# Kernel tuning notes

Measured on AMD Instinct MI355X. Metric: run time of the kernel, lower is better.

## Reference

```python
import jax, jax.numpy as jnp
import numpy as np
import math

FOV, NEAR, FAR = 60.0, 0.1, 100.0
W_RES, H_RES = 128, 128
N_GAUSS = 1024


def _normalize(v):
    return v / (jnp.linalg.norm(v) + 1e-8)


def _view_matrix(pos, look_at, up):
    # Same construction as Camera._compute_view_matrix
    f = _normalize(look_at - pos)
    r = _normalize(jnp.cross(f, up))
    u = _normalize(jnp.cross(r, f))
    return jnp.stack([
        jnp.concatenate([r, -jnp.dot(r, pos)[None]]),
        jnp.concatenate([u, -jnp.dot(u, pos)[None]]),
        jnp.concatenate([-f, jnp.dot(f, pos)[None]]),
        jnp.array([0.0, 0.0, 0.0, 1.0], dtype=pos.dtype),
    ])


def _proj_matrix():
    # Same construction as Camera._compute_projection_matrix
    aspect = W_RES / H_RES
    foc = 1.0 / math.tan(math.radians(FOV) / 2.0)
    P = np.zeros((4, 4), np.float32)
    P[0, 0] = foc / aspect
    P[1, 1] = foc
    P[2, 2] = (FAR + NEAR) / (NEAR - FAR)
    P[2, 3] = 2.0 * FAR * NEAR / (NEAR - FAR)
    P[3, 2] = -1.0
    return jnp.asarray(P)


def _quat_to_rot(q):
    # q: [N,4] (w,x,y,z) -> [N,3,3]
    q = q / (jnp.linalg.norm(q, axis=-1, keepdims=True) + 1e-8)
    w, x, y, z = q[:, 0], q[:, 1], q[:, 2], q[:, 3]
    return jnp.stack([
        jnp.stack([1 - 2 * (y * y + z * z), 2 * (x * y - w * z), 2 * (x * z + w * y)], -1),
        jnp.stack([2 * (x * y + w * z), 1 - 2 * (x * x + z * z), 2 * (y * z - w * x)], -1),
        jnp.stack([2 * (x * z - w * y), 2 * (y * z + w * x), 1 - 2 * (x * x + y * y)], -1),
    ], axis=1)


def _splat(means, log_scales, quats, opacity_logits, colors, cam_position, look_at, up):
    V = _view_matrix(cam_position, look_at, up)
    P = _proj_matrix()

    # 3D covariance: R S S^T R^T
    R = _quat_to_rot(quats)                       # [N,3,3]
    S = jnp.exp(log_scales)                       # [N,3]
    M = R * S[:, None, :]
    cov3d = jnp.einsum('nij,nkj->nik', M, M)      # [N,3,3]

    # Project means to view / clip / pixel space
    mh = jnp.concatenate([means, jnp.ones((means.shape[0], 1), means.dtype)], -1)
    pv = mh @ V.T                                 # [N,4] view space
    tx, ty, tz = pv[:, 0], pv[:, 1], pv[:, 2]     # tz < 0 in front of camera
    depth = -tz
    clip = pv @ P.T
    cw = jnp.where(jnp.abs(clip[:, 3]) < 1e-6, 1e-6, clip[:, 3])
    ndc = clip[:, :2] / cw[:, None]
    px = (ndc[:, 0] + 1.0) * 0.5 * W_RES          # pixel x center
    py = (ndc[:, 1] + 1.0) * 0.5 * H_RES          # pixel y center

    # EWA Jacobian -> 2D covariance
    foc = 1.0 / math.tan(math.radians(FOV) / 2.0)
    fx = foc / (W_RES / H_RES) * (W_RES / 2.0)
    fy = foc * (H_RES / 2.0)
    zsafe = jnp.where(jnp.abs(tz) < 1e-6, 1e-6, tz)
    zero = jnp.zeros_like(zsafe)
    J = jnp.stack([
        jnp.stack([fx / zsafe, zero, -fx * tx / (zsafe * zsafe)], -1),
        jnp.stack([zero, fy / zsafe, -fy * ty / (zsafe * zsafe)], -1),
    ], axis=1)                                    # [N,2,3]
    T = jnp.einsum('nij,jk->nik', J, V[:3, :3])   # [N,2,3]
    cov2d = jnp.einsum('nij,njk,nlk->nil', T, cov3d, T)  # [N,2,2]
    a = cov2d[:, 0, 0] + 0.3
    b = cov2d[:, 0, 1]
    c = cov2d[:, 1, 1] + 0.3
    det = jnp.maximum(a * c - b * b, 1e-6)
    ia, ib, ic = c / det, -b / det, a / det       # inverse 2x2

    # Per-pixel Gaussian weights: [N,H,W]
    u = jnp.arange(W_RES, dtype=means.dtype) + 0.5
    v = jnp.arange(H_RES, dtype=means.dtype) + 0.5
    dx = px[:, None, None] - u[None, None, :]
    dy = py[:, None, None] - v[None, :, None]
    power = -0.5 * (ia[:, None, None] * dx * dx
                    + 2.0 * ib[:, None, None] * dx * dy
                    + ic[:, None, None] * dy * dy)
    opac = jax.nn.sigmoid(opacity_logits)
    w = opac[:, None, None] * jnp.exp(jnp.minimum(power, 0.0))
    valid = (depth > NEAR) & (depth < FAR)
    w = jnp.where(valid[:, None, None], w, 0.0)
    w = jnp.clip(w, 0.0, 0.99)

    # Depth sort (front-to-back) then alpha composite via exclusive cumsum of log(1-a)
    order = jnp.argsort(depth)
    ws = w[order]                                 # [N,H,W]
    cs = jax.nn.sigmoid(colors)[order]            # [N,3]
    ds = depth[order]
    log_om = jnp.log1p(-ws)
    trans = jnp.exp(jnp.cumsum(log_om, axis=0) - log_om)  # exclusive transmittance
    contrib = trans * ws                          # [N,H,W]
    rgb = jnp.einsum('nhw,nc->chw', contrib, cs)  # [3,H,W]
    depth_img = jnp.sum(contrib * ds[:, None, None], axis=0, keepdims=True)
    alpha_img = jnp.sum(contrib, axis=0, keepdims=True)
    # background_color = [0,0,0] so no background term is added
    return rgb, depth_img, alpha_img


def setup_inputs() -> dict:
    key = jax.random.key(0)
    ks = jax.random.split(key, 6)
    means = jax.random.normal(ks[0], (N_GAUSS, 3), jnp.float32) * 1.5
    log_scales = jax.random.normal(ks[1], (N_GAUSS, 3), jnp.float32) * 0.3 - 2.5
    quats = jax.random.normal(ks[2], (N_GAUSS, 4), jnp.float32)
    opacity_logits = jax.random.normal(ks[3], (N_GAUSS,), jnp.float32)
    colors = jax.random.normal(ks[4], (N_GAUSS, 3), jnp.float32)
    cam_position = jnp.array([0.0, 0.0, 5.0], jnp.float32) + 0.05 * jax.random.normal(ks[5], (3,), jnp.float32)
    look_at = jnp.zeros((3,), jnp.float32)
    up = jnp.array([0.0, 1.0, 0.0], jnp.float32)
    return {"means": means, "log_scales": log_scales, "quats": quats,
            "opacity_logits": opacity_logits, "colors": colors,
            "cam_position": cam_position, "look_at": look_at, "up": up}


def reference(means, log_scales, quats, opacity_logits, colors, cam_position, look_at, up):
    return _splat(means, log_scales, quats, opacity_logits, colors, cam_position, look_at, up)
```

## Files before the change

kernel.cpp:

```cpp
#include <hip/hip_runtime.h>
#include <math.h>

#define NG 1024
#define W_RES 128
#define H_RES 128
#define NPIX (W_RES * H_RES)
#define NCHUNK 8
#define CH (NG / NCHUNK)

__device__ float g_sorted[NG * 12];
__device__ float g_part[6 * NCHUNK * NPIX];

__global__ __launch_bounds__(1024) void prep_sort_kernel(
    const float* __restrict__ means, const float* __restrict__ log_scales,
    const float* __restrict__ quats, const float* __restrict__ opacity_logits,
    const float* __restrict__ colors, const float* __restrict__ cam,
    const float* __restrict__ look, const float* __restrict__ up) {
  __shared__ float sp[NG * 12];
  __shared__ float skey[NG];
  __shared__ int sval[NG];
  const int t = threadIdx.x;

  const float cpx = cam[0], cpy = cam[1], cpz = cam[2];
  float fx0 = look[0] - cpx, fy0 = look[1] - cpy, fz0 = look[2] - cpz;
  float inv = 1.f / (sqrtf(fx0 * fx0 + fy0 * fy0 + fz0 * fz0) + 1e-8f);
  const float fX = fx0 * inv, fY = fy0 * inv, fZ = fz0 * inv;
  const float ux0 = up[0], uy0 = up[1], uz0 = up[2];
  float rX0 = fY * uz0 - fZ * uy0, rY0 = fZ * ux0 - fX * uz0, rZ0 = fX * uy0 - fY * ux0;
  inv = 1.f / (sqrtf(rX0 * rX0 + rY0 * rY0 + rZ0 * rZ0) + 1e-8f);
  const float rX = rX0 * inv, rY = rY0 * inv, rZ = rZ0 * inv;
  float uX0 = rY * fZ - rZ * fY, uY0 = rZ * fX - rX * fZ, uZ0 = rX * fY - rY * fX;
  inv = 1.f / (sqrtf(uX0 * uX0 + uY0 * uY0 + uZ0 * uZ0) + 1e-8f);
  const float uX = uX0 * inv, uY = uY0 * inv, uZ = uZ0 * inv;
  const float V00 = rX, V01 = rY, V02 = rZ, V03 = -(rX * cpx + rY * cpy + rZ * cpz);
  const float V10 = uX, V11 = uY, V12 = uZ, V13 = -(uX * cpx + uY * cpy + uZ * cpz);
  const float V20 = -fX, V21 = -fY, V22 = -fZ, V23 = (fX * cpx + fY * cpy + fZ * cpz);

  const float foc = 1.7320508075688772f;
  const float fpx = foc * 64.f;
  const float fpy = foc * 64.f;

  {
    float qw = quats[4 * t + 0], qx = quats[4 * t + 1], qy = quats[4 * t + 2], qz = quats[4 * t + 3];
    float qinv = 1.f / (sqrtf(qw * qw + qx * qx + qy * qy + qz * qz) + 1e-8f);
    qw *= qinv; qx *= qinv; qy *= qinv; qz *= qinv;
    const float R00 = 1.f - 2.f * (qy * qy + qz * qz), R01 = 2.f * (qx * qy - qw * qz), R02 = 2.f * (qx * qz + qw * qy);
    const float R10 = 2.f * (qx * qy + qw * qz), R11 = 1.f - 2.f * (qx * qx + qz * qz), R12 = 2.f * (qy * qz - qw * qx);
    const float R20 = 2.f * (qx * qz - qw * qy), R21 = 2.f * (qy * qz + qw * qx), R22 = 1.f - 2.f * (qx * qx + qy * qy);
    const float s0 = __expf(log_scales[3 * t + 0]);
    const float s1 = __expf(log_scales[3 * t + 1]);
    const float s2 = __expf(log_scales[3 * t + 2]);
    const float M00 = R00 * s0, M01 = R01 * s1, M02 = R02 * s2;
    const float M10 = R10 * s0, M11 = R11 * s1, M12 = R12 * s2;
    const float M20 = R20 * s0, M21 = R21 * s1, M22 = R22 * s2;
    const float c00 = M00 * M00 + M01 * M01 + M02 * M02;
    const float c01 = M00 * M10 + M01 * M11 + M02 * M12;
    const float c02 = M00 * M20 + M01 * M21 + M02 * M22;
    const float c11 = M10 * M10 + M11 * M11 + M12 * M12;
    const float c12 = M10 * M20 + M11 * M21 + M12 * M22;
    const float c22 = M20 * M20 + M21 * M21 + M22 * M22;
    const float mx = means[3 * t + 0], my = means[3 * t + 1], mz = means[3 * t + 2];
    const float tx = V00 * mx + V01 * my + V02 * mz + V03;
    const float ty = V10 * mx + V11 * my + V12 * mz + V13;
    const float tz = V20 * mx + V21 * my + V22 * mz + V23;
    const float depth = -tz;
    const float cw = (fabsf(depth) < 1e-6f) ? 1e-6f : depth;
    const float pxs = (foc * tx / cw + 1.f) * 0.5f * (float)W_RES;
    const float pys = (foc * ty / cw + 1.f) * 0.5f * (float)H_RES;
    const float zs = (fabsf(tz) < 1e-6f) ? 1e-6f : tz;
    const float J00 = fpx / zs, J02 = -fpx * tx / (zs * zs);
    const float J11 = fpy / zs, J12 = -fpy * ty / (zs * zs);
    const float T00 = J00 * V00 + J02 * V20;
    const float T01 = J00 * V01 + J02 * V21;
    const float T02 = J00 * V02 + J02 * V22;
    const float T10 = J11 * V10 + J12 * V20;
    const float T11 = J11 * V11 + J12 * V21;
    const float T12 = J11 * V12 + J12 * V22;
    const float t00 = T00 * c00 + T01 * c01 + T02 * c02;
    const float t01 = T00 * c01 + T01 * c11 + T02 * c12;
    const float t02 = T00 * c02 + T01 * c12 + T02 * c22;
    const float t10 = T10 * c00 + T11 * c01 + T12 * c02;
    const float t11 = T10 * c01 + T11 * c11 + T12 * c12;
    const float t12 = T10 * c02 + T11 * c12 + T12 * c22;
    const float a = t00 * T00 + t01 * T01 + t02 * T02 + 0.3f;
    const float bb = t00 * T10 + t01 * T11 + t02 * T12;
    const float c = t10 * T10 + t11 * T11 + t12 * T12 + 0.3f;
    const float det = fmaxf(a * c - bb * bb, 1e-6f);
    const float ia = c / det, ib = -bb / det, ic = a / det;
    float op = 1.f / (1.f + __expf(-opacity_logits[t]));
    const bool valid = (depth > 0.1f) && (depth < 100.f);
    if (!valid) op = 0.f;
    const float cr = 1.f / (1.f + __expf(-colors[3 * t + 0]));
    const float cg = 1.f / (1.f + __expf(-colors[3 * t + 1]));
    const float cb = 1.f / (1.f + __expf(-colors[3 * t + 2]));
    float* s = sp + t * 12;
    s[0] = pxs; s[1] = pys; s[2] = ia; s[3] = ib; s[4] = ic; s[5] = op;
    s[6] = cr;  s[7] = cg;  s[8] = cb; s[9] = depth; s[10] = 0.f; s[11] = 0.f;
    skey[t] = depth;
    sval[t] = t;
  }
  __syncthreads();

  for (int k = 2; k <= NG; k <<= 1) {
    for (int j = k >> 1; j > 0; j >>= 1) {
      const int ixj = t ^ j;
      if (ixj > t) {
        const float ka = skey[t], kb = skey[ixj];
        const bool asc = ((t & k) == 0);
        if (asc ? (ka > kb) : (ka < kb)) {
          skey[t] = kb; skey[ixj] = ka;
          const int va = sval[t]; sval[t] = sval[ixj]; sval[ixj] = va;
        }
      }
      __syncthreads();
    }
  }

  {
    const int src = sval[t];
    const float* s = sp + src * 12;
    float* d = g_sorted + t * 12;
#pragma unroll
    for (int k2 = 0; k2 < 12; ++k2) d[k2] = s[k2];
  }
}

__global__ __launch_bounds__(256) void render_chunk_kernel() {
  const int p = blockIdx.x * 256 + threadIdx.x;
  const int chunk = blockIdx.y;
  const float u = (float)(p & (W_RES - 1)) + 0.5f;
  const float v = (float)(p >> 7) + 0.5f;
  const float* __restrict__ g = g_sorted + chunk * CH * 12;
  float T = 1.f, ar = 0.f, ag = 0.f, ab = 0.f, ad = 0.f, aa = 0.f;
#pragma unroll 4
  for (int n = 0; n < CH; ++n) {
    const float gpx = g[n * 12 + 0], gpy = g[n * 12 + 1];
    const float ia = g[n * 12 + 2], ib = g[n * 12 + 3], ic = g[n * 12 + 4];
    const float op = g[n * 12 + 5];
    const float cr = g[n * 12 + 6], cg = g[n * 12 + 7], cb = g[n * 12 + 8];
    const float dep = g[n * 12 + 9];
    const float dx = gpx - u, dy = gpy - v;
    float pw = -0.5f * (ia * dx * dx + 2.f * ib * dx * dy + ic * dy * dy);
    pw = fminf(pw, 0.f);
    const float w = fminf(op * __expf(pw), 0.99f);
    const float ctr = T * w;
    ar += ctr * cr; ag += ctr * cg; ab += ctr * cb;
    ad += ctr * dep; aa += ctr;
    T *= (1.f - w);
  }
  const int idx = chunk * NPIX + p;
  g_part[0 * NCHUNK * NPIX + idx] = ar;
  g_part[1 * NCHUNK * NPIX + idx] = ag;
  g_part[2 * NCHUNK * NPIX + idx] = ab;
  g_part[3 * NCHUNK * NPIX + idx] = ad;
  g_part[4 * NCHUNK * NPIX + idx] = aa;
  g_part[5 * NCHUNK * NPIX + idx] = T;
}

__global__ __launch_bounds__(256) void combine_kernel(float* __restrict__ out) {
  const int p = blockIdx.x * 256 + threadIdx.x;
  float T = 1.f, r = 0.f, g = 0.f, b = 0.f, d = 0.f, a = 0.f;
#pragma unroll
  for (int ch = 0; ch < NCHUNK; ++ch) {
    const int idx = ch * NPIX + p;
    const float pr = g_part[0 * NCHUNK * NPIX + idx];
    const float pg = g_part[1 * NCHUNK * NPIX + idx];
    const float pb = g_part[2 * NCHUNK * NPIX + idx];
    const float pd = g_part[3 * NCHUNK * NPIX + idx];
    const float pa = g_part[4 * NCHUNK * NPIX + idx];
    const float pT = g_part[5 * NCHUNK * NPIX + idx];
    r += T * pr; g += T * pg; b += T * pb; d += T * pd; a += T * pa;
    T *= pT;
  }
  out[0 * NPIX + p] = r;
  out[1 * NPIX + p] = g;
  out[2 * NPIX + p] = b;
  out[3 * NPIX + p] = d;
  out[4 * NPIX + p] = a;
}

extern "C" void kernel_launch(void* const* d_in, const int* in_sizes, int n_in,
                              void* d_out, int out_size, void* d_ws, size_t ws_size,
                              hipStream_t stream) {
  const float* means = (const float*)d_in[0];
  const float* log_scales = (const float*)d_in[1];
  const float* quats = (const float*)d_in[2];
  const float* opacity_logits = (const float*)d_in[3];
  const float* colors = (const float*)d_in[4];
  const float* cam = (const float*)d_in[5];
  const float* look = (const float*)d_in[6];
  const float* up = (const float*)d_in[7];
  float* out = (float*)d_out;

  prep_sort_kernel<<<1, 1024, 0, stream>>>(means, log_scales, quats, opacity_logits,
                                           colors, cam, look, up);
  render_chunk_kernel<<<dim3(NPIX / 256, NCHUNK), 256, 0, stream>>>();
  combine_kernel<<<NPIX / 256, 256, 0, stream>>>(out);
}
```

Before: 105.3 us.

## Replace bitonic sort with rank sort and add per-tile gaussian culling

The single-block bitonic sort is replaced by a multi-block rank computation, where each thread counts how many gaussians have smaller depth and scatters its parameters to that rank in SoA/float4 layout. Rendering switches to 16x16 pixel tiles. Each block culls its chunk's gaussians against the tile using a radius derived from the largest eigenvalue and opacity, so only survivors are blended. Log-opacity is folded into the exponent, which drops contributions below about 1e-7 and slightly changes the numerics.

After: 106.9 us. About the same (+1.5%).

```diff
diff --git a/kernel.cpp b/kernel.cpp
--- a/kernel.cpp
+++ b/kernel.cpp
@@ -7,19 +7,26 @@
 #define NPIX (W_RES * H_RES)
 #define NCHUNK 8
 #define CH (NG / NCHUNK)
-
-__device__ float g_sorted[NG * 12];
-__device__ float g_part[6 * NCHUNK * NPIX];
-
-__global__ __launch_bounds__(1024) void prep_sort_kernel(
+#define TILES_X 8
+#define TILES_Y 8
+#define NTILE (TILES_X * TILES_Y)
+
+__device__ float  s_px[NG];
+__device__ float  s_py[NG];
+__device__ float  s_R2[NG];
+__device__ float4 s_g0[NG];
+__device__ float4 s_g1[NG];
+__device__ float4 s_col[NG];
+__device__ float  g_part[6 * NCHUNK * NPIX];
+
+__global__ __launch_bounds__(128) void prep_kernel(
     const float* __restrict__ means, const float* __restrict__ log_scales,
     const float* __restrict__ quats, const float* __restrict__ opacity_logits,
     const float* __restrict__ colors, const float* __restrict__ cam,
     const float* __restrict__ look, const float* __restrict__ up) {
-  __shared__ float sp[NG * 12];
-  __shared__ float skey[NG];
-  __shared__ int sval[NG];
-  const int t = threadIdx.x;
+  __shared__ __align__(16) float sdepth[NG];
+  const int tid = threadIdx.x;
+  const int me = blockIdx.x * CH + tid;
 
   const float cpx = cam[0], cpy = cam[1], cpz = cam[2];
   float fx0 = look[0] - cpx, fy0 = look[1] - cpy, fz0 = look[2] - cpz;
@@ -40,114 +47,144 @@
   const float fpx = foc * 64.f;
   const float fpy = foc * 64.f;
 
-  {
-    float qw = quats[4 * t + 0], qx = quats[4 * t + 1], qy = quats[4 * t + 2], qz = quats[4 * t + 3];
-    float qinv = 1.f / (sqrtf(qw * qw + qx * qx + qy * qy + qz * qz) + 1e-8f);
-    qw *= qinv; qx *= qinv; qy *= qinv; qz *= qinv;
-    const float R00 = 1.f - 2.f * (qy * qy + qz * qz), R01 = 2.f * (qx * qy - qw * qz), R02 = 2.f * (qx * qz + qw * qy);
-    const float R10 = 2.f * (qx * qy + qw * qz), R11 = 1.f - 2.f * (qx * qx + qz * qz), R12 = 2.f * (qy * qz - qw * qx);
-    const float R20 = 2.f * (qx * qz - qw * qy), R21 = 2.f * (qy * qz + qw * qx), R22 = 1.f - 2.f * (qx * qx + qy * qy);
-    const float s0 = __expf(log_scales[3 * t + 0]);
-    const float s1 = __expf(log_scales[3 * t + 1]);
-    const float s2 = __expf(log_scales[3 * t + 2]);
-    const float M00 = R00 * s0, M01 = R01 * s1, M02 = R02 * s2;
-    const float M10 = R10 * s0, M11 = R11 * s1, M12 = R12 * s2;
-    const float M20 = R20 * s0, M21 = R21 * s1, M22 = R22 * s2;
-    const float c00 = M00 * M00 + M01 * M01 + M02 * M02;
-    const float c01 = M00 * M10 + M01 * M11 + M02 * M12;
-    const float c02 = M00 * M20 + M01 * M21 + M02 * M22;
-    const float c11 = M10 * M10 + M11 * M11 + M12 * M12;
-    const float c12 = M10 * M20 + M11 * M21 + M12 * M22;
-    const float c22 = M20 * M20 + M21 * M21 + M22 * M22;
-    const float mx = means[3 * t + 0], my = means[3 * t + 1], mz = means[3 * t + 2];
-    const float tx = V00 * mx + V01 * my + V02 * mz + V03;
-    const float ty = V10 * mx + V11 * my + V12 * mz + V13;
-    const float tz = V20 * mx + V21 * my + V22 * mz + V23;
-    const float depth = -tz;
-    const float cw = (fabsf(depth) < 1e-6f) ? 1e-6f : depth;
-    const float pxs = (foc * tx / cw + 1.f) * 0.5f * (float)W_RES;
-    const float pys = (foc * ty / cw + 1.f) * 0.5f * (float)H_RES;
-    const float zs = (fabsf(tz) < 1e-6f) ? 1e-6f : tz;
-    const float J00 = fpx / zs, J02 = -fpx * tx / (zs * zs);
-    const float J11 = fpy / zs, J12 = -fpy * ty / (zs * zs);
-    const float T00 = J00 * V00 + J02 * V20;
-    const float T01 = J00 * V01 + J02 * V21;
-    const float T02 = J00 * V02 + J02 * V22;
-    const float T10 = J11 * V10 + J12 * V20;
-    const float T11 = J11 * V11 + J12 * V21;
-    const float T12 = J11 * V12 + J12 * V22;
-    const float t00 = T00 * c00 + T01 * c01 + T02 * c02;
-    const float t01 = T00 * c01 + T01 * c11 + T02 * c12;
-    const float t02 = T00 * c02 + T01 * c12 + T02 * c22;
-    const float t10 = T10 * c00 + T11 * c01 + T12 * c02;
-    const float t11 = T10 * c01 + T11 * c11 + T12 * c12;
-    const float t12 = T10 * c02 + T11 * c12 + T12 * c22;
-    const float a = t00 * T00 + t01 * T01 + t02 * T02 + 0.3f;
-    const float bb = t00 * T10 + t01 * T11 + t02 * T12;
-    const float c = t10 * T10 + t11 * T11 + t12 * T12 + 0.3f;
-    const float det = fmaxf(a * c - bb * bb, 1e-6f);
-    const float ia = c / det, ib = -bb / det, ic = a / det;
-    float op = 1.f / (1.f + __expf(-opacity_logits[t]));
-    const bool valid = (depth > 0.1f) && (depth < 100.f);
-    if (!valid) op = 0.f;
-    const float cr = 1.f / (1.f + __expf(-colors[3 * t + 0]));
-    const float cg = 1.f / (1.f + __expf(-colors[3 * t + 1]));
-    const float cb = 1.f / (1.f + __expf(-colors[3 * t + 2]));
-    float* s = sp + t * 12;
-    s[0] = pxs; s[1] = pys; s[2] = ia; s[3] = ib; s[4] = ic; s[5] = op;
-    s[6] = cr;  s[7] = cg;  s[8] = cb; s[9] = depth; s[10] = 0.f; s[11] = 0.f;
-    skey[t] = depth;
-    sval[t] = t;
+#pragma unroll
+  for (int i = 0; i < NG / CH; ++i) {
+    const int g = i * CH + tid;
+    const float mx = means[3 * g + 0], my = means[3 * g + 1], mz = means[3 * g + 2];
+    sdepth[g] = -(V20 * mx + V21 * my + V22 * mz + V23);
   }
   __syncthreads();
 
-  for (int k = 2; k <= NG; k <<= 1) {
-    for (int j = k >> 1; j > 0; j >>= 1) {
-      const int ixj = t ^ j;
-      if (ixj > t) {
-        const float ka = skey[t], kb = skey[ixj];
-        const bool asc = ((t & k) == 0);
-        if (asc ? (ka > kb) : (ka < kb)) {
-          skey[t] = kb; skey[ixj] = ka;
-          const int va = sval[t]; sval[t] = sval[ixj]; sval[ixj] = va;
-        }
-      }
-      __syncthreads();
-    }
-  }
-
-  {
-    const int src = sval[t];
-    const float* s = sp + src * 12;
-    float* d = g_sorted + t * 12;
-#pragma unroll
-    for (int k2 = 0; k2 < 12; ++k2) d[k2] = s[k2];
-  }
-}
-
-__global__ __launch_bounds__(256) void render_chunk_kernel() {
-  const int p = blockIdx.x * 256 + threadIdx.x;
+  const float dme = sdepth[me];
+  int rank = 0;
+  const float4* dep4 = (const float4*)sdepth;
+#pragma unroll 4
+  for (int k = 0; k < NG / 4; ++k) {
+    const float4 d4 = dep4[k];
+    const int j = 4 * k;
+    rank += (d4.x < dme || (d4.x == dme && (j + 0) < me)) ? 1 : 0;
+    rank += (d4.y < dme || (d4.y == dme && (j + 1) < me)) ? 1 : 0;
+    rank += (d4.z < dme || (d4.z == dme && (j + 2) < me)) ? 1 : 0;
+    rank += (d4.w < dme || (d4.w == dme && (j + 3) < me)) ? 1 : 0;
+  }
+
+  float qw = quats[4 * me + 0], qx = quats[4 * me + 1], qy = quats[4 * me + 2], qz = quats[4 * me + 3];
+  float qinv = 1.f / (sqrtf(qw * qw + qx * qx + qy * qy + qz * qz) + 1e-8f);
+  qw *= qinv; qx *= qinv; qy *= qinv; qz *= qinv;
+  const float R00 = 1.f - 2.f * (qy * qy + qz * qz), R01 = 2.f * (qx * qy - qw * qz), R02 = 2.f * (qx * qz + qw * qy);
+  const float R10 = 2.f * (qx * qy + qw * qz), R11 = 1.f - 2.f * (qx * qx + qz * qz), R12 = 2.f * (qy * qz - qw * qx);
+  const float R20 = 2.f * (qx * qz - qw * qy), R21 = 2.f * (qy * qz + qw * qx), R22 = 1.f - 2.f * (qx * qx + qy * qy);
+  const float s0 = __expf(log_scales[3 * me + 0]);
+  const float s1 = __expf(log_scales[3 * me + 1]);
+  const float s2 = __expf(log_scales[3 * me + 2]);
+  const float M00 = R00 * s0, M01 = R01 * s1, M02 = R02 * s2;
+  const float M10 = R10 * s0, M11 = R11 * s1, M12 = R12 * s2;
+  const float M20 = R20 * s0, M21 = R21 * s1, M22 = R22 * s2;
+  const float c00 = M00 * M00 + M01 * M01 + M02 * M02;
+  const float c01 = M00 * M10 + M01 * M11 + M02 * M12;
+  const float c02 = M00 * M20 + M01 * M21 + M02 * M22;
+  const float c11 = M10 * M10 + M11 * M11 + M12 * M12;
+  const float c12 = M10 * M20 + M11 * M21 + M12 * M22;
+  const float c22 = M20 * M20 + M21 * M21 + M22 * M22;
+  const float mx = means[3 * me + 0], my = means[3 * me + 1], mz = means[3 * me + 2];
+  const float tx = V00 * mx + V01 * my + V02 * mz + V03;
+  const float ty = V10 * mx + V11 * my + V12 * mz + V13;
+  const float tz = V20 * mx + V21 * my + V22 * mz + V23;
+  const float depth = -tz;
+  const float cw = (fabsf(depth) < 1e-6f) ? 1e-6f : depth;
+  const float pxs = (foc * tx / cw + 1.f) * 0.5f * (float)W_RES;
+  const float pys = (foc * ty / cw + 1.f) * 0.5f * (float)H_RES;
+  const float zs = (fabsf(tz) < 1e-6f) ? 1e-6f : tz;
+  const float J00 = fpx / zs, J02 = -fpx * tx / (zs * zs);
+  const float J11 = fpy / zs, J12 = -fpy * ty / (zs * zs);
+  const float T00 = J00 * V00 + J02 * V20;
+  const float T01 = J00 * V01 + J02 * V21;
+  const float T02 = J00 * V02 + J02 * V22;
+  const float T10 = J11 * V10 + J12 * V20;
+  const float T11 = J11 * V11 + J12 * V21;
+  const float T12 = J11 * V12 + J12 * V22;
+  const float t00 = T00 * c00 + T01 * c01 + T02 * c02;
+  const float t01 = T00 * c01 + T01 * c11 + T02 * c12;
+  const float t02 = T00 * c02 + T01 * c12 + T02 * c22;
+  const float t10 = T10 * c00 + T11 * c01 + T12 * c02;
+  const float t11 = T10 * c01 + T11 * c11 + T12 * c12;
+  const float t12 = T10 * c02 + T11 * c12 + T12 * c22;
+  const float a  = t00 * T00 + t01 * T01 + t02 * T02 + 0.3f;
+  const float bb = t00 * T10 + t01 * T11 + t02 * T12;
+  const float c  = t10 * T10 + t11 * T11 + t12 * T12 + 0.3f;
+  const float det = fmaxf(a * c - bb * bb, 1e-6f);
+  const float ia = c / det, ib = -bb / det, ic = a / det;
+  const float op = 1.f / (1.f + __expf(-opacity_logits[me]));
+  const bool valid = (depth > 0.1f) && (depth < 100.f);
+  const float lam = 0.5f * (a + c) + sqrtf(0.25f * (a - c) * (a - c) + bb * bb);
+  float R2v = 2.f * lam * logf(op * 1e7f);
+  if (!valid) R2v = -1.f;
+  const float logop = logf(op);
+  const float cr = 1.f / (1.f + __expf(-colors[3 * me + 0]));
+  const float cg = 1.f / (1.f + __expf(-colors[3 * me + 1]));
+  const float cb = 1.f / (1.f + __expf(-colors[3 * me + 2]));
+
+  s_px[rank] = pxs;
+  s_py[rank] = pys;
+  s_R2[rank] = R2v;
+  s_g0[rank] = make_float4(pxs, pys, -0.5f * ia, -ib);
+  s_g1[rank] = make_float4(-0.5f * ic, logop, depth, 0.f);
+  s_col[rank] = make_float4(cr, cg, cb, 0.f);
+}
+
+__global__ __launch_bounds__(256) void render_kernel() {
+  __shared__ int slist[CH];
+  __shared__ int scnt[2];
+  __shared__ int stotal;
+  const int tid = threadIdx.x;
+  const int tile = blockIdx.x;
   const int chunk = blockIdx.y;
-  const float u = (float)(p & (W_RES - 1)) + 0.5f;
-  const float v = (float)(p >> 7) + 0.5f;
-  const float* __restrict__ g = g_sorted + chunk * CH * 12;
+  const int ox = (tile & (TILES_X - 1)) * 16;
+  const int oy = (tile >> 3) * 16;
+  const float x0 = ox + 0.5f, x1 = ox + 15.5f;
+  const float y0 = oy + 0.5f, y1 = oy + 15.5f;
+
+  bool surv = false;
+  if (tid < CH) {
+    const int g = chunk * CH + tid;
+    const float gx = s_px[g], gy = s_py[g], r2 = s_R2[g];
+    const float nx = fminf(fmaxf(gx, x0), x1);
+    const float ny = fminf(fmaxf(gy, y0), y1);
+    const float ddx = nx - gx, ddy = ny - gy;
+    surv = (ddx * ddx + ddy * ddy) <= r2;
+  }
+  const unsigned long long m = __ballot(surv);
+  const int wid = tid >> 6, lane = tid & 63;
+  if (tid < CH && lane == 0) scnt[wid] = __popcll(m);
+  __syncthreads();
+  if (surv) {
+    const int base = (wid == 1) ? scnt[0] : 0;
+    const int pos = base + __popcll(m & ((1ull << lane) - 1ull));
+    slist[pos] = chunk * CH + tid;
+  }
+  if (tid == 0) stotal = scnt[0] + scnt[1];
+  __syncthreads();
+  const int ns = stotal;
+
+  const int lx = tid & 15, ly = tid >> 4;
+  const float u = (float)(ox + lx) + 0.5f;
+  const float v = (float)(oy + ly) + 0.5f;
   float T = 1.f, ar = 0.f, ag = 0.f, ab = 0.f, ad = 0.f, aa = 0.f;
-#pragma unroll 4
-  for (int n = 0; n < CH; ++n) {
-    const float gpx = g[n * 12 + 0], gpy = g[n * 12 + 1];
-    const float ia = g[n * 12 + 2], ib = g[n * 12 + 3], ic = g[n * 12 + 4];
-    const float op = g[n * 12 + 5];
-    const float cr = g[n * 12 + 6], cg = g[n * 12 + 7], cb = g[n * 12 + 8];
-    const float dep = g[n * 12 + 9];
-    const float dx = gpx - u, dy = gpy - v;
-    float pw = -0.5f * (ia * dx * dx + 2.f * ib * dx * dy + ic * dy * dy);
-    pw = fminf(pw, 0.f);
-    const float w = fminf(op * __expf(pw), 0.99f);
+  for (int s = 0; s < ns; ++s) {
+    const int g = slist[s];
+    const float4 g0 = s_g0[g];
+    const float4 g1 = s_g1[g];
+    const float4 cc = s_col[g];
+    const float dx = g0.x - u, dy = g0.y - v;
+    float pw = dx * (g0.z * dx + g0.w * dy) + g1.x * dy * dy;
+    pw = fminf(pw, 0.f) + g1.y;
+    const float w = fminf(__expf(pw), 0.99f);
     const float ctr = T * w;
-    ar += ctr * cr; ag += ctr * cg; ab += ctr * cb;
-    ad += ctr * dep; aa += ctr;
+    ar += ctr * cc.x; ag += ctr * cc.y; ab += ctr * cc.z;
+    ad += ctr * g1.z; aa += ctr;
     T *= (1.f - w);
   }
+  const int p = (oy + ly) * W_RES + (ox + lx);
   const int idx = chunk * NPIX + p;
   g_part[0 * NCHUNK * NPIX + idx] = ar;
   g_part[1 * NCHUNK * NPIX + idx] = ag;
@@ -192,8 +229,8 @@
   const float* up = (const float*)d_in[7];
   float* out = (float*)d_out;
 
-  prep_sort_kernel<<<1, 1024, 0, stream>>>(means, log_scales, quats, opacity_logits,
-                                           colors, cam, look, up);
-  render_chunk_kernel<<<dim3(NPIX / 256, NCHUNK), 256, 0, stream>>>();
+  prep_kernel<<<NCHUNK, CH, 0, stream>>>(means, log_scales, quats, opacity_logits,
+                                         colors, cam, look, up);
+  render_kernel<<<dim3(NTILE, NCHUNK), 256, 0, stream>>>();
   combine_kernel<<<NPIX / 256, 256, 0, stream>>>(out);
 }
```
